# Performance work log

Measured on AMD Instinct MI355X. Metric: run time of the kernel, lower is better.

## Reference

```python
import jax, jax.numpy as jnp
import numpy as np

B, C, H, W = 2, 256, 56, 56
NH = 8
HD = C // NH
SCALE = HD ** -0.5
BN_EPS = 1e-5


def _linear(x, w, b=None):
    y = jnp.einsum('...i,oi->...o', x, w)
    return y + b if b is not None else y


def _dwconv3(v, w, b):
    # depthwise 3x3, stride 1, pad 1
    y = jax.lax.conv_general_dilated(v, w, (1, 1), 'SAME',
                                     dimension_numbers=('NCHW', 'OIHW', 'NCHW'),
                                     feature_group_count=C)
    return y + b[None, :, None, None]


def _spectral(x, context, qw, kvw, pw, pb, dww, dwb):
    # SpectralCrossAttention, sr_ratio=1 path
    xt = jnp.transpose(x, (0, 2, 3, 1))                    # B,H,W,C
    q = jnp.transpose(_linear(xt, qw), (0, 3, 1, 2))       # B,C,H,W
    ct = jnp.transpose(context, (0, 2, 3, 1))
    kv = _linear(ct, kvw)                                  # B,H,W,2C -> split [2,C]
    k = jnp.transpose(kv[..., :C], (0, 3, 1, 2))
    v = jnp.transpose(kv[..., C:], (0, 3, 1, 2))
    v_local = _dwconv3(v, dww, dwb)
    qf = jnp.fft.rfft2(q, s=(H, W), axes=(-2, -1), norm='ortho')
    kf = jnp.fft.rfft2(k, s=(H, W), axes=(-2, -1), norm='ortho')
    attn_map = jnp.fft.irfft2(qf * kf, s=(H, W), axes=(-2, -1), norm='ortho')
    out = attn_map * v + v_local
    out = _linear(jnp.transpose(out, (0, 2, 3, 1)), pw, pb)
    return jnp.transpose(out, (0, 3, 1, 2))


def _token(x, context, qw, kvw, pw, pb, cw):
    # TokenSpectralResidualCrossAttention, sr_ratio=1 path (de_conv = Identity)
    N = H * W
    xt = jnp.transpose(x.reshape(B, C, N), (0, 2, 1))       # B,N,C
    ct = jnp.transpose(context.reshape(B, C, N), (0, 2, 1))
    q = jnp.transpose(_linear(xt, qw).reshape(B, N, NH, HD), (0, 2, 1, 3))  # B,NH,N,HD
    kv = _linear(ct, kvw).reshape(B, N, 2, NH, HD)
    k = jnp.transpose(kv[:, :, 0], (0, 2, 1, 3))
    v = jnp.transpose(kv[:, :, 1], (0, 2, 1, 3))            # B,NH,N,HD
    attn = jax.nn.softmax(jnp.einsum('bhnd,bhmd->bhnm', q, k) * SCALE, axis=-1)
    x_attn = jnp.transpose(jnp.einsum('bhnm,bhmd->bhnd', attn, v), (0, 2, 1, 3)).reshape(B, N, C)
    v_img = jnp.transpose(v, (0, 1, 3, 2)).reshape(B, C, H, W)
    vf = jnp.fft.rfft2(v_img, s=(H, W), axes=(-2, -1), norm='ortho')
    weight = cw[..., 0] + 1j * cw[..., 1]                   # C,H,W//2+1 complex
    v_res = jnp.fft.irfft2(vf * weight[None], s=(H, W), axes=(-2, -1), norm='ortho')
    v_res = jnp.transpose(v_res.reshape(B, C, N), (0, 2, 1))
    out = _linear(x_attn + v_res, pw, pb)
    return jnp.transpose(out, (0, 2, 1)).reshape(B, C, H, W)


def _fuse(os_, ot, g_w1, g_bn_g, g_bn_b, g_w2, g_b2):
    # spatial_gate: Conv1x1(2C->C, no bias) -> BN(eval: mean0/var1) -> ReLU -> Conv1x1(C->1) -> Sigmoid
    g_in = jnp.concatenate([os_, ot], axis=1)               # B,2C,H,W
    h = jnp.einsum('oc,bchw->bohw', g_w1, g_in)
    h = h / jnp.sqrt(1.0 + BN_EPS) * g_bn_g[None, :, None, None] + g_bn_b[None, :, None, None]
    h = jax.nn.relu(h)
    gate = jax.nn.sigmoid(jnp.einsum('oc,bchw->bohw', g_w2, h) + g_b2[None, :, None, None])
    return gate * os_ + (1.0 - gate) * ot


def setup_inputs():
    key = jax.random.key(0)
    ks = jax.random.split(key, 14)
    p = lambda i, shape, s=0.02: jax.random.normal(ks[i], shape, jnp.float32) * s
    return {
        'x': jax.random.normal(ks[0], (B, C, H, W), jnp.float32),
        'context': jax.random.normal(ks[1], (B, C, H, W), jnp.float32),
        's_q_w': p(2, (C, C)),
        's_kv_w': p(3, (2 * C, C)),
        's_proj_w': p(4, (C, C)),
        's_proj_b': jnp.zeros((C,), jnp.float32),
        's_dw_w': p(5, (C, 1, 3, 3), float(np.sqrt(2.0 / 9.0))),
        's_dw_b': jnp.zeros((C,), jnp.float32),
        't_q_w': p(6, (C, C)),
        't_kv_w': p(7, (2 * C, C)),
        't_proj_w': p(8, (C, C)),
        't_proj_b': jnp.zeros((C,), jnp.float32),
        't_cw': p(9, (C, H, W // 2 + 1, 2)),
        'g_w1': p(10, (C, 2 * C), float(np.sqrt(2.0 / C))),
        'g_bn_g': jnp.ones((C,), jnp.float32),
        'g_bn_b': jnp.zeros((C,), jnp.float32),
        'g_w2': p(11, (1, C), float(np.sqrt(2.0 / C))),
        'g_b2': jnp.zeros((1,), jnp.float32),
    }


def reference(x, context, s_q_w, s_kv_w, s_proj_w, s_proj_b, s_dw_w, s_dw_b,
              t_q_w, t_kv_w, t_proj_w, t_proj_b, t_cw,
              g_w1, g_bn_g, g_bn_b, g_w2, g_b2):
    os_ = _spectral(x, context, s_q_w, s_kv_w, s_proj_w, s_proj_b, s_dw_w, s_dw_b)
    ot = _token(x, context, t_q_w, t_kv_w, t_proj_w, t_proj_b, t_cw)
    return _fuse(os_, ot, g_w1, g_bn_g, g_bn_b, g_w2, g_b2)
```

## Files before the change

kernel.cpp:

```cpp
#include <hip/hip_runtime.h>

namespace {
constexpr int kB = 2;
constexpr int kC = 256;
constexpr int kH = 56;
constexpr int kW = 56;
constexpr int kN = kH * kW;
constexpr int kNH = 8;
constexpr int kHD = 32;
constexpr int kNF = kW / 2 + 1;
constexpr int kSpec = kH * kNF;
constexpr long kCN = (long)kC * kN;
constexpr float kAttScale = 0.17677669529663687f;
constexpr float kLog2e = 1.4426950408889634f;
constexpr float kAng = 6.283185307179586f / 56.0f;
constexpr int TW1F = 0;
constexpr int TW2F = 8192;
constexpr int TW1I = 12288;
constexpr int TW2I = 20480;
constexpr int TWTOT = 24576;
}

typedef __attribute__((ext_vector_type(8))) short short8;
typedef __attribute__((ext_vector_type(4))) float float4v;

union Frag {
    short8 s;
    unsigned short u[8];
    uint2 u2[2];
    uint4 u4;
};

__device__ __forceinline__ unsigned short f2b(float f) {
    unsigned u = __float_as_uint(f);
    return (unsigned short)((u + 0x7FFFu + ((u >> 16) & 1u)) >> 16);
}
__device__ __forceinline__ unsigned f2b_pk(float a, float b) {
    unsigned ua = __float_as_uint(a); ua = (ua + 0x7FFFu + ((ua >> 16) & 1u)) >> 16;
    unsigned ub = __float_as_uint(b); ub = (ub + 0x7FFFu + ((ub >> 16) & 1u)) >> 16;
    return ua | (ub << 16);
}
__device__ __forceinline__ unsigned pk_trunc(float a, float b) {
    return (__float_as_uint(a) >> 16) | (__float_as_uint(b) & 0xFFFF0000u);
}
__device__ __forceinline__ uint4 pk8(const float* v) {
    return make_uint4(f2b_pk(v[0], v[1]), f2b_pk(v[2], v[3]),
                      f2b_pk(v[4], v[5]), f2b_pk(v[6], v[7]));
}

__global__ __launch_bounds__(256)
void twiddle_init_kernel(unsigned short* __restrict__ tw)
{
    int idx = blockIdx.x * 256 + threadIdx.x;
    if (idx >= TWTOT) return;
    float val = 0.f;
    if (idx < TW2F) {
        int r = idx >> 6, c = idx & 63;
        if (c < 56) {
            if (r < 56)       val = cosf(kAng * (float)((r * c) % 56));
            else if (r < 112) val = sinf(kAng * (float)(((r - 56) * c) % 56));
        }
    } else if (idx < TW1I) {
        int t = idx - TW2F; int r = t >> 6, c = t & 63;
        if (c < 56) {
            if (r < 29)                  val = cosf(kAng * (float)((r * c) % 56));
            else if (r >= 32 && r < 61)  val = sinf(kAng * (float)(((r - 32) * c) % 56));
        }
    } else if (idx < TW2I) {
        int t = idx - TW1I; int r = t >> 6, c = t & 63;
        if (c < 56) {
            if (r < 56)                  val = cosf(kAng * (float)((r * c) % 56));
            else if (r >= 64 && r < 120) val = sinf(kAng * (float)(((r - 64) * c) % 56));
        }
    } else {
        int t = idx - TW2I; int x = t >> 6, c = t & 63;
        if (x < 56 && c < 58) {
            int v = c >> 1;
            float wv = ((v == 0) || (v == 28)) ? 1.f : 2.f;
            float a = kAng * (float)((v * x) % 56);
            val = (c & 1) ? (-wv * sinf(a)) : (wv * cosf(a));
        }
    }
    tw[idx] = f2b(val);
}

__device__ void dft_fwd_body(char* smem, int bx,
                             const float* __restrict__ s0, const float* __restrict__ s1,
                             const float* __restrict__ s2, float* __restrict__ d0,
                             float* __restrict__ d1, float* __restrict__ d2,
                             const unsigned short* __restrict__ tw)
{
    const int which = bx >> 9, ch = bx & 511;
    const int b = ch >> 8, c = ch & 255;
    const float* src; long stride; float* spec;
    if (which == 0)      { src = s0; stride = kCN;     spec = d0; }
    else if (which == 1) { src = s1; stride = 2 * kCN; spec = d1; }
    else                 { src = s2; stride = 2 * kCN; spec = d2; }
    const float* img = src + (long)b * stride + (long)c * kN;

    unsigned short (*Gb)[72]   = (unsigned short(*)[72])smem;
    unsigned short (*imgT)[72] = (unsigned short(*)[72])(smem + 18432);
    float (*Yb)[116]           = (float(*)[116])(smem + 18432);

    const int tid = threadIdx.x;
    const int wave = tid >> 6, lane = tid & 63;
    const int ln = lane & 15, qd = lane >> 4;

    for (int i = tid; i < 64 * 72; i += 256) {
        int r = i / 72, cc = i - r * 72;
        if (r >= 56 || cc >= 56) imgT[r][cc] = 0;
    }
    for (int i = tid; i < kN; i += 256) {
        int y = i / 56, x = i - y * 56;
        imgT[x][y] = f2b(img[i]);
    }
    __syncthreads();

    float4v acc1[2][4];
#pragma unroll
    for (int m = 0; m < 2; ++m)
#pragma unroll
        for (int n = 0; n < 4; ++n) acc1[m][n] = (float4v){0.f, 0.f, 0.f, 0.f};
#pragma unroll
    for (int ks = 0; ks < 2; ++ks) {
        Frag a[2], bf[4];
#pragma unroll
        for (int m = 0; m < 2; ++m)
            a[m].u4 = *(const uint4*)(tw + TW1F + ((2 * wave + m) * 16 + ln) * 64 + ks * 32 + qd * 8);
#pragma unroll
        for (int n = 0; n < 4; ++n)
            bf[n].u4 = *(const uint4*)&imgT[n * 16 + ln][ks * 32 + qd * 8];
#pragma unroll
        for (int m = 0; m < 2; ++m)
#pragma unroll
            for (int n = 0; n < 4; ++n)
                acc1[m][n] = __builtin_amdgcn_mfma_f32_16x16x32_bf16(a[m].s, bf[n].s, acc1[m][n], 0, 0, 0);
    }
#pragma unroll
    for (int m = 0; m < 2; ++m)
#pragma unroll
        for (int n = 0; n < 4; ++n)
#pragma unroll
            for (int r = 0; r < 4; ++r)
                Gb[(2 * wave + m) * 16 + qd * 4 + r][n * 16 + ln] = f2b(acc1[m][n][r]);
    __syncthreads();

    float4v acc2[7];
#pragma unroll
    for (int n = 0; n < 7; ++n) acc2[n] = (float4v){0.f, 0.f, 0.f, 0.f};
#pragma unroll
    for (int ks = 0; ks < 2; ++ks) {
        Frag a;
        a.u4 = *(const uint4*)(tw + TW2F + (wave * 16 + ln) * 64 + ks * 32 + qd * 8);
#pragma unroll
        for (int n = 0; n < 7; ++n) {
            Frag bb;
            bb.u4 = *(const uint4*)&Gb[n * 16 + ln][ks * 32 + qd * 8];
            acc2[n] = __builtin_amdgcn_mfma_f32_16x16x32_bf16(a.s, bb.s, acc2[n], 0, 0, 0);
        }
    }
#pragma unroll
    for (int n = 0; n < 7; ++n)
#pragma unroll
        for (int r = 0; r < 4; ++r)
            Yb[wave * 16 + qd * 4 + r][n * 16 + ln] = acc2[n][r];
    __syncthreads();

    float2* outp = (float2*)spec + (long)ch * kSpec;
    for (int i = tid; i < kSpec; i += 256) {
        int u = i / kNF, v = i - u * kNF;
        float Qr = Yb[v][u] - Yb[32 + v][56 + u];
        float Qi = -Yb[32 + v][u] - Yb[v][56 + u];
        outp[i] = make_float2(Qr, Qi);
    }
}

__device__ void prepack_body(char* smem, int blk, const float* __restrict__ tkv,
                             unsigned short* __restrict__ Kp,
                             unsigned short* __restrict__ Vp)
{
    const int i = blk % 49;
    const int h = (blk / 49) & 7;
    const int b = blk / (49 * 8);
    const float* kb = tkv + (long)b * 2 * kCN + (long)h * kHD * kN;
    const float* vb = kb + kCN;
    const int tid = threadIdx.x;

    float (*Ks)[72] = (float(*)[72])smem;
#pragma unroll
    for (int j = 0; j < 8; ++j) {
        int e = tid + j * 256;
        int d = e >> 6, c = e & 63;
        Ks[d][c] = kb[(long)d * kN + i * 64 + c];
    }
    __syncthreads();
    {
        int tl = tid >> 6, lnn = (tid >> 2) & 15, qdd = tid & 3;
        float v[8];
#pragma unroll
        for (int j = 0; j < 8; ++j) v[j] = Ks[qdd * 8 + j][tl * 16 + lnn];
        unsigned short* dst = Kp + ((long)(b * 8 + h) * 196 + 4 * i + tl) * 512 + lnn * 32 + qdd * 8;
        *(uint4*)dst = pk8(v);
    }
    {
        int g = tid >> 7, dh = (tid >> 6) & 1, lnn = (tid >> 2) & 15, qdd = tid & 3;
        int d = dh * 16 + lnn;
        const float* src = vb + (long)d * kN + i * 64 + g * 32 + qdd * 8;
        float v[8];
        *(float4*)&v[0] = *(const float4*)src;
        *(float4*)&v[4] = *(const float4*)(src + 4);
        unsigned short* dst = Vp + ((long)(b * 8 + h) * 49 + i) * 2048 + ((g * 2 + dh) * 16 + lnn) * 32 + qdd * 8;
        *(uint4*)dst = pk8(v);
    }
}

__global__ __launch_bounds__(256)
void fwd3_prepack_kernel(const float* __restrict__ s0, const float* __restrict__ s1,
                         const float* __restrict__ s2, float* __restrict__ d0,
                         float* __restrict__ d1, float* __restrict__ d2,
                         const unsigned short* __restrict__ tw,
                         const float* __restrict__ tkv,
                         unsigned short* __restrict__ Kp, unsigned short* __restrict__ Vp)
{
    __shared__ __align__(16) char smem[48128];
    if (blockIdx.x < 1536)
        dft_fwd_body(smem, blockIdx.x, s0, s1, s2, d0, d1, d2, tw);
    else
        prepack_body(smem, blockIdx.x - 1536, tkv, Kp, Vp);
}

__global__ __launch_bounds__(256)
void dft_inv_mfma2(const float* __restrict__ fQ, const float* __restrict__ fK,
                   const float* __restrict__ fV, const float* __restrict__ cw,
                   float* __restrict__ dst1, float* __restrict__ dst2,
                   const float* __restrict__ skvp, const float* __restrict__ dww,
                   const float* __restrict__ dwb, const unsigned short* __restrict__ tw)
{
    const int unit = blockIdx.x >> 9;
    const int ch = blockIdx.x & 511;
    const int b = ch >> 8, c = ch & 255;
    __shared__ __align__(16) char smem[41984];
    unsigned short (*Pb)[72] = (unsigned short(*)[72])smem;
    float (*Yb)[64]          = (float(*)[64])(smem + 9216);
    unsigned short (*T2)[72] = (unsigned short(*)[72])smem;
    float (*svs)[65]         = (float(*)[65])(smem + 9216);

    const int tid = threadIdx.x;
    const int wave = tid >> 6, lane = tid & 63;
    const int ln = lane & 15, qd = lane >> 4;

    const float2* Pin; const float2* Min; float scale; float* dst;
    if (unit == 0) {
        Pin = (const float2*)fQ + (long)ch * kSpec;
        Min = (const float2*)fK + (long)ch * kSpec;
        scale = 1.0f / 175616.0f; dst = dst1;
    } else {
        Pin = (const float2*)fV + (long)ch * kSpec;
        Min = (const float2*)cw + (long)c * kSpec;
        scale = 1.0f / 3136.0f; dst = dst2;
    }

    for (int i = tid; i < 64 * 72; i += 256) {
        int r = i / 72, cc = i - r * 72;
        if (r >= 58 || cc >= 56) Pb[r][cc] = 0;
    }
    for (int i = tid; i < kSpec; i += 256) {
        int u = i / kNF, v = i - u * kNF;
        float2 p = Pin[i];
        float2 m = Min[i];
        float pr = (p.x * m.x - p.y * m.y) * scale;
        float pi = (p.x * m.y + p.y * m.x) * scale;
        Pb[2 * v][u]     = f2b(pr);
        Pb[2 * v + 1][u] = f2b(pi);
    }
    __syncthreads();

    float4v acc1[2][4];
#pragma unroll
    for (int m = 0; m < 2; ++m)
#pragma unroll
        for (int n = 0; n < 4; ++n) acc1[m][n] = (float4v){0.f, 0.f, 0.f, 0.f};
#pragma unroll
    for (int ks = 0; ks < 2; ++ks) {
        Frag a[2], bf[4];
#pragma unroll
        for (int m = 0; m < 2; ++m)
            a[m].u4 = *(const uint4*)(tw + TW1I + ((2 * wave + m) * 16 + ln) * 64 + ks * 32 + qd * 8);
#pragma unroll
        for (int n = 0; n < 4; ++n)
            bf[n].u4 = *(const uint4*)&Pb[n * 16 + ln][ks * 32 + qd * 8];
#pragma unroll
        for (int m = 0; m < 2; ++m)
#pragma unroll
            for (int n = 0; n < 4; ++n)
                acc1[m][n] = __builtin_amdgcn_mfma_f32_16x16x32_bf16(a[m].s, bf[n].s, acc1[m][n], 0, 0, 0);
    }
#pragma unroll
    for (int m = 0; m < 2; ++m)
#pragma unroll
        for (int n = 0; n < 4; ++n)
#pragma unroll
            for (int r = 0; r < 4; ++r)
                Yb[(2 * wave + m) * 16 + qd * 4 + r][n * 16 + ln] = acc1[m][n][r];
    __syncthreads();

    for (int i = tid; i < 64 * 72; i += 256) {
        int r = i / 72, cc = i - r * 72;
        if (r >= 56 || cc >= 58) T2[r][cc] = 0;
    }
    __syncthreads();
    for (int i = tid; i < 56 * kNF; i += 256) {
        int y = i / kNF, v = i - y * kNF;
        float Tr = Yb[y][2 * v]     - Yb[64 + y][2 * v + 1];
        float Ti = Yb[y][2 * v + 1] + Yb[64 + y][2 * v];
        T2[y][2 * v]     = f2b(Tr);
        T2[y][2 * v + 1] = f2b(Ti);
    }
    __syncthreads();

    float wreg[9]; float bias = 0.f;
    if (unit == 0) {
        const float* svp = skvp + (long)b * 2 * kCN + kCN + (long)c * kN;
        for (int i = tid; i < 58 * 65; i += 256) {
            int y = i / 65, x = i - y * 65;
            if (y == 0 || y == 57 || x == 0 || x >= 57) ((float*)svs)[i] = 0.f;
        }
        for (int i = tid; i < kN; i += 256) {
            int y = i / 56, x = i - y * 56;
            svs[y + 1][x + 1] = svp[i];
        }
#pragma unroll
        for (int j = 0; j < 9; ++j) wreg[j] = dww[c * 9 + j];
        bias = dwb[c];
    }

    float4v acc2[4];
#pragma unroll
    for (int n = 0; n < 4; ++n) acc2[n] = (float4v){0.f, 0.f, 0.f, 0.f};
#pragma unroll
    for (int ks = 0; ks < 2; ++ks) {
        Frag a;
        a.u4 = *(const uint4*)(tw + TW2I + (wave * 16 + ln) * 64 + ks * 32 + qd * 8);
#pragma unroll
        for (int n = 0; n < 4; ++n) {
            Frag bb;
            bb.u4 = *(const uint4*)&T2[n * 16 + ln][ks * 32 + qd * 8];
            acc2[n] = __builtin_amdgcn_mfma_f32_16x16x32_bf16(a.s, bb.s, acc2[n], 0, 0, 0);
        }
    }
    __syncthreads();

    float* outd = dst + (long)ch * kN;
#pragma unroll
    for (int n = 0; n < 4; ++n) {
        int y = n * 16 + ln;
        if (y < 56) {
#pragma unroll
            for (int r = 0; r < 4; ++r) {
                int x = wave * 16 + qd * 4 + r;
                if (x < 56) {
                    int e = y * 56 + x;
                    if (unit == 0) {
                        float s = bias;
                        s = fmaf(wreg[0], svs[y][x],     s);
                        s = fmaf(wreg[1], svs[y][x + 1], s);
                        s = fmaf(wreg[2], svs[y][x + 2], s);
                        s = fmaf(wreg[3], svs[y + 1][x],     s);
                        s = fmaf(wreg[4], svs[y + 1][x + 1], s);
                        s = fmaf(wreg[5], svs[y + 1][x + 2], s);
                        s = fmaf(wreg[6], svs[y + 2][x],     s);
                        s = fmaf(wreg[7], svs[y + 2][x + 1], s);
                        s = fmaf(wreg[8], svs[y + 2][x + 2], s);
                        outd[e] = fmaf(acc2[n][r], svs[y + 1][x + 1], s);
                    } else {
                        outd[e] = acc2[n][r];
                    }
                }
            }
        }
    }
}

__global__ __launch_bounds__(256)
void gemm_fused(const float* __restrict__ W0, const float* __restrict__ W1,
                const float* __restrict__ X0, const float* __restrict__ X1,
                const float* __restrict__ b0, const float* __restrict__ b1,
                float* __restrict__ Y0, float* __restrict__ Y1,
                int oHalf, int CI, long xbs, long ybs, int oOffset)
{
    const int b  = blockIdx.z;
    const int sel = blockIdx.y >= oHalf;
    const int o0 = (sel ? blockIdx.y - oHalf : blockIdx.y) * 64;
    const int oY = o0 + (sel ? oOffset : 0);
    const int n0 = blockIdx.x * 128;
    const float* Wm = sel ? W1 : W0;
    const float* bias = sel ? b1 : b0;
    const float* Xb = (sel ? X1 : X0) + (long)b * xbs;
    float* Yb = (sel ? Y1 : Y0) + (long)b * ybs;

    __shared__ __align__(16) unsigned short Wt[64][40];
    __shared__ __align__(16) unsigned short Xt[128][40];

    const int tid = threadIdx.x;
    const int wave = tid >> 6, lane = tid & 63;
    const int ln = lane & 15, qd = lane >> 4;
    const int wy = wave >> 1, wx = wave & 1;

    const int ow = tid >> 2, kcw = tid & 3;
    const int nx = tid & 127, kcx = tid >> 7;
    const bool xvalid = (n0 + nx) < kN;

    float4v acc[2][4];
#pragma unroll
    for (int i = 0; i < 2; ++i)
#pragma unroll
        for (int j = 0; j < 4; ++j) acc[i][j] = (float4v){0.f, 0.f, 0.f, 0.f};

    float wpre[8], xpre[16];
    {
        const float* ws = Wm + (long)(o0 + ow) * CI + kcw * 8;
        *(float4*)&wpre[0] = *(const float4*)ws;
        *(float4*)&wpre[4] = *(const float4*)(ws + 4);
#pragma unroll
        for (int j = 0; j < 16; ++j)
            xpre[j] = xvalid ? Xb[(long)(kcx * 16 + j) * kN + n0 + nx] : 0.f;
    }

    for (int k0 = 0; k0 < CI; k0 += 32) {
        *(uint4*)&Wt[ow][kcw * 8]      = pk8(wpre);
        *(uint4*)&Xt[nx][kcx * 16]     = pk8(xpre);
        *(uint4*)&Xt[nx][kcx * 16 + 8] = pk8(xpre + 8);
        __syncthreads();

        if (k0 + 32 < CI) {
            const float* ws = Wm + (long)(o0 + ow) * CI + k0 + 32 + kcw * 8;
            *(float4*)&wpre[0] = *(const float4*)ws;
            *(float4*)&wpre[4] = *(const float4*)(ws + 4);
#pragma unroll
            for (int j = 0; j < 16; ++j)
                xpre[j] = xvalid ? Xb[(long)(k0 + 32 + kcx * 16 + j) * kN + n0 + nx] : 0.f;
        }

        Frag af[2], bf4[4];
#pragma unroll
        for (int mt = 0; mt < 2; ++mt)
            af[mt].u4 = *(const uint4*)&Wt[wy * 32 + mt * 16 + ln][qd * 8];
#pragma unroll
        for (int nt = 0; nt < 4; ++nt)
            bf4[nt].u4 = *(const uint4*)&Xt[wx * 64 + nt * 16 + ln][qd * 8];
#pragma unroll
        for (int mt = 0; mt < 2; ++mt)
#pragma unroll
            for (int nt = 0; nt < 4; ++nt)
                acc[mt][nt] = __builtin_amdgcn_mfma_f32_16x16x32_bf16(
                    af[mt].s, bf4[nt].s, acc[mt][nt], 0, 0, 0);
        __syncthreads();
    }

#pragma unroll
    for (int mt = 0; mt < 2; ++mt) {
        const int obL = o0 + wy * 32 + mt * 16 + qd * 4;
        const int obY = oY + wy * 32 + mt * 16 + qd * 4;
#pragma unroll
        for (int nt = 0; nt < 4; ++nt) {
            const int n = n0 + wx * 64 + nt * 16 + ln;
            if (n < kN) {
#pragma unroll
                for (int r = 0; r < 4; ++r) {
                    float v = acc[mt][nt][r];
                    if (bias) v += bias[obL + r];
                    Yb[(long)(obY + r) * kN + n] = v;
                }
            }
        }
    }
}

__global__ __launch_bounds__(256)
void gemm_bn_kernel(const float* __restrict__ Wm, const float* __restrict__ X,
                    const float* __restrict__ gamma, const float* __restrict__ beta,
                    float* __restrict__ Y, int CI, long xbs, long ybs)
{
    const int b  = blockIdx.z;
    const int o0 = blockIdx.y * 64;
    const int n0 = blockIdx.x * 128;
    const float* Xb = X + (long)b * xbs;
    float* Yb = Y + (long)b * ybs;

    __shared__ __align__(16) unsigned short Wt[64][40];
    __shared__ __align__(16) unsigned short Xt[128][40];

    const int tid = threadIdx.x;
    const int wave = tid >> 6, lane = tid & 63;
    const int ln = lane & 15, qd = lane >> 4;
    const int wy = wave >> 1, wx = wave & 1;

    const int ow = tid >> 2, kcw = tid & 3;
    const int nx = tid & 127, kcx = tid >> 7;
    const bool xvalid = (n0 + nx) < kN;

    float4v acc[2][4];
#pragma unroll
    for (int i = 0; i < 2; ++i)
#pragma unroll
        for (int j = 0; j < 4; ++j) acc[i][j] = (float4v){0.f, 0.f, 0.f, 0.f};

    float wpre[8], xpre[16];
    {
        const float* ws = Wm + (long)(o0 + ow) * CI + kcw * 8;
        *(float4*)&wpre[0] = *(const float4*)ws;
        *(float4*)&wpre[4] = *(const float4*)(ws + 4);
#pragma unroll
        for (int j = 0; j < 16; ++j)
            xpre[j] = xvalid ? Xb[(long)(kcx * 16 + j) * kN + n0 + nx] : 0.f;
    }

    for (int k0 = 0; k0 < CI; k0 += 32) {
        *(uint4*)&Wt[ow][kcw * 8]      = pk8(wpre);
        *(uint4*)&Xt[nx][kcx * 16]     = pk8(xpre);
        *(uint4*)&Xt[nx][kcx * 16 + 8] = pk8(xpre + 8);
        __syncthreads();

        if (k0 + 32 < CI) {
            const float* ws = Wm + (long)(o0 + ow) * CI + k0 + 32 + kcw * 8;
            *(float4*)&wpre[0] = *(const float4*)ws;
            *(float4*)&wpre[4] = *(const float4*)(ws + 4);
#pragma unroll
            for (int j = 0; j < 16; ++j)
                xpre[j] = xvalid ? Xb[(long)(k0 + 32 + kcx * 16 + j) * kN + n0 + nx] : 0.f;
        }

        Frag af[2], bf4[4];
#pragma unroll
        for (int mt = 0; mt < 2; ++mt)
            af[mt].u4 = *(const uint4*)&Wt[wy * 32 + mt * 16 + ln][qd * 8];
#pragma unroll
        for (int nt = 0; nt < 4; ++nt)
            bf4[nt].u4 = *(const uint4*)&Xt[wx * 64 + nt * 16 + ln][qd * 8];
#pragma unroll
        for (int mt = 0; mt < 2; ++mt)
#pragma unroll
            for (int nt = 0; nt < 4; ++nt)
                acc[mt][nt] = __builtin_amdgcn_mfma_f32_16x16x32_bf16(
                    af[mt].s, bf4[nt].s, acc[mt][nt], 0, 0, 0);
        __syncthreads();
    }

    const float rs = rsqrtf(1.0f + 1e-5f);
#pragma unroll
    for (int mt = 0; mt < 2; ++mt) {
        const int ob = o0 + wy * 32 + mt * 16 + qd * 4;
#pragma unroll
        for (int nt = 0; nt < 4; ++nt) {
            const int n = n0 + wx * 64 + nt * 16 + ln;
            if (n < kN) {
#pragma unroll
                for (int r = 0; r < 4; ++r) {
                    const int o = ob + r;
                    float v = fmaxf(fmaf(acc[mt][nt][r], gamma[o] * rs, beta[o]), 0.f);
                    Yb[(long)o * kN + n] = v;
                }
            }
        }
    }
}

__global__ __launch_bounds__(256, 4)
void attn_mfma_kernel(const float* __restrict__ tq,
                      const unsigned short* __restrict__ Kp,
                      const unsigned short* __restrict__ Vp,
                      float* __restrict__ Op, float* __restrict__ lp)
{
    const int b = blockIdx.z >> 2, sp = blockIdx.z & 3;
    const int h = blockIdx.y;
    const int q0 = blockIdx.x * 128;
    const int tid = threadIdx.x;
    const int wave = tid >> 6, lane = tid & 63;
    const int qd = lane >> 4, ln = lane & 15;
    const int i0 = (sp == 0) ? 0 : (12 * sp + 1);
    const int i1 = 12 * sp + 13;

    const float* qb = tq + (long)b * kCN + (long)h * kHD * kN;
    const unsigned short* KpB = Kp + (long)(b * 8 + h) * 196 * 512 + ln * 32 + qd * 8;
    const unsigned short* VpB = Vp + (long)(b * 8 + h) * 49 * 2048 + ln * 32 + qd * 8;

    __shared__ __align__(16) unsigned short Ps[4][32 * 40];
    unsigned short* PsW = Ps[wave];

    const float qscale = kAttScale * kLog2e;
    Frag qf[2];
#pragma unroll
    for (int qt = 0; qt < 2; ++qt) {
        int qg = q0 + wave * 32 + qt * 16 + ln;
        bool qv = qg < kN;
#pragma unroll
        for (int j = 0; j < 8; ++j) {
            int d = qd * 8 + j;
            float v = qv ? qb[(long)d * kN + qg] * qscale : 0.f;
            qf[qt].u[j] = f2b(v);
        }
    }

    float4v o[2][2];
#pragma unroll
    for (int qt = 0; qt < 2; ++qt)
#pragma unroll
        for (int dh = 0; dh < 2; ++dh) o[qt][dh] = (float4v){0.f, 0.f, 0.f, 0.f};
    float lsum[2] = {0.f, 0.f};

    unsigned W[4][2][2];
    Frag ka[4];
#pragma unroll
    for (int m = 0; m < 4; ++m)
        ka[m].u4 = *(const uint4*)(KpB + (long)(4 * i0 + m) * 512);

    auto computeW = [&]() {
#pragma unroll
        for (int m = 0; m < 4; ++m) {
            float4v s0 = __builtin_amdgcn_mfma_f32_16x16x32_bf16(
                ka[m].s, qf[0].s, (float4v){0.f, 0.f, 0.f, 0.f}, 0, 0, 0);
            float4v s1 = __builtin_amdgcn_mfma_f32_16x16x32_bf16(
                ka[m].s, qf[1].s, (float4v){0.f, 0.f, 0.f, 0.f}, 0, 0, 0);
            float a0 = __builtin_amdgcn_exp2f(s0[0]);
            float a1 = __builtin_amdgcn_exp2f(s0[1]);
            float a2 = __builtin_amdgcn_exp2f(s0[2]);
            float a3 = __builtin_amdgcn_exp2f(s0[3]);
            lsum[0] += (a0 + a1) + (a2 + a3);
            W[m][0][0] = pk_trunc(a0, a1);
            W[m][0][1] = pk_trunc(a2, a3);
            float b0 = __builtin_amdgcn_exp2f(s1[0]);
            float b1 = __builtin_amdgcn_exp2f(s1[1]);
            float b2 = __builtin_amdgcn_exp2f(s1[2]);
            float b3 = __builtin_amdgcn_exp2f(s1[3]);
            lsum[1] += (b0 + b1) + (b2 + b3);
            W[m][1][0] = pk_trunc(b0, b1);
            W[m][1][1] = pk_trunc(b2, b3);
        }
    };

    computeW();
    if (i0 + 1 < i1) {
#pragma unroll
        for (int m = 0; m < 4; ++m)
            ka[m].u4 = *(const uint4*)(KpB + (long)(4 * (i0 + 1) + m) * 512);
    }

    for (int i = i0; i < i1; ++i) {
        Frag va[2][2];
#pragma unroll
        for (int g = 0; g < 2; ++g)
#pragma unroll
            for (int dh = 0; dh < 2; ++dh)
                va[g][dh].u4 = *(const uint4*)(VpB + (long)i * 2048 + (g * 2 + dh) * 512);

#pragma unroll
        for (int m = 0; m < 4; ++m)
#pragma unroll
            for (int qt = 0; qt < 2; ++qt)
                *(uint2*)&PsW[(qt * 16 + ln) * 40 + m * 16 + qd * 4] =
                    make_uint2(W[m][qt][0], W[m][qt][1]);

        if (i + 1 < i1) {
            computeW();
            if (i + 2 < i1) {
#pragma unroll
                for (int m = 0; m < 4; ++m)
                    ka[m].u4 = *(const uint4*)(KpB + (long)(4 * (i + 2) + m) * 512);
            }
        }

#pragma unroll
        for (int g = 0; g < 2; ++g) {
            Frag pa[2];
#pragma unroll
            for (int qt = 0; qt < 2; ++qt)
                pa[qt].u4 = *(const uint4*)&PsW[(qt * 16 + ln) * 40 + g * 32 + qd * 8];
#pragma unroll
            for (int qt = 0; qt < 2; ++qt)
#pragma unroll
                for (int dh = 0; dh < 2; ++dh)
                    o[qt][dh] = __builtin_amdgcn_mfma_f32_16x16x32_bf16(
                        pa[qt].s, va[g][dh].s, o[qt][dh], 0, 0, 0);
        }
    }

    const long grp = (long)(sp * 16 + b * 8 + h);
#pragma unroll
    for (int qt = 0; qt < 2; ++qt) {
        lsum[qt] += __shfl_xor(lsum[qt], 16, 64);
        lsum[qt] += __shfl_xor(lsum[qt], 32, 64);
        if (qd == 0)
            lp[grp * 3200 + q0 + wave * 32 + qt * 16 + ln] = lsum[qt];
#pragma unroll
        for (int dh = 0; dh < 2; ++dh)
#pragma unroll
            for (int r = 0; r < 4; ++r) {
                int q = q0 + wave * 32 + qt * 16 + qd * 4 + r;
                Op[(grp * 3200 + q) * 32 + dh * 16 + ln] = o[qt][dh][r];
            }
    }
}

__global__ __launch_bounds__(256)
void attn_combine_kernel(const float* __restrict__ Op, const float* __restrict__ lp,
                         float* __restrict__ xo)
{
    const int qc = blockIdx.x, bh = blockIdx.y;
    const int b = bh >> 3, h = bh & 7;
    const int q0 = qc * 64;
    __shared__ float T[32][65];
    const int tid = threadIdx.x;

    for (int i = tid; i < 64 * 32; i += 256) {
        int ql = i >> 5, d = i & 31;
        float ov = 0.f, l = 0.f;
#pragma unroll
        for (int s = 0; s < 4; ++s) {
            long g = (long)(s * 16 + bh);
            ov += Op[(g * 3200 + q0 + ql) * 32 + d];
            l  += lp[g * 3200 + q0 + ql];
        }
        T[d][ql] = ov / l;
    }
    __syncthreads();
    for (int i = tid; i < 32 * 64; i += 256) {
        int d = i >> 6, ql = i & 63;
        xo[(long)b * kCN + (long)(h * kHD + d) * kN + q0 + ql] += T[d][ql];
    }
}

__global__ __launch_bounds__(256)
void gateblend_kernel(const float* __restrict__ hbuf, const float* __restrict__ w2,
                      const float* __restrict__ b2, const float* __restrict__ gcat,
                      float* __restrict__ out)
{
    const int n0 = blockIdx.x * 64;
    const int b = blockIdx.y;
    const int lane = threadIdx.x & 63;
    const int g = threadIdx.x >> 6;
    const float* hb = hbuf + (long)b * kCN + n0 + lane;
    float s = 0.f;
#pragma unroll 8
    for (int c = g * 64; c < g * 64 + 64; ++c)
        s = fmaf(w2[c], hb[(long)c * kN], s);
    __shared__ float red[4][64];
    __shared__ float sgate[64];
    red[g][lane] = s;
    __syncthreads();
    if (g == 0) {
        float t = red[0][lane] + red[1][lane] + red[2][lane] + red[3][lane];
        sgate[lane] = 1.f / (1.f + __expf(-(t + b2[0])));
    }
    __syncthreads();
    const float gt = sgate[lane];
    const float* osp = gcat + (long)b * 2 * kCN + n0 + lane;
    const float* otp = osp + kCN;
    float* op = out + (long)b * kCN + n0 + lane;
    for (int c = g; c < kC; c += 4) {
        float os = osp[(long)c * kN];
        float ot = otp[(long)c * kN];
        op[(long)c * kN] = gt * os + (1.f - gt) * ot;
    }
}

extern "C" void kernel_launch(void* const* d_in, const int* in_sizes, int n_in,
                              void* d_out, int out_size, void* d_ws, size_t ws_size,
                              hipStream_t stream)
{
    const float* x      = (const float*)d_in[0];
    const float* ctx    = (const float*)d_in[1];
    const float* s_q_w  = (const float*)d_in[2];
    const float* s_kv_w = (const float*)d_in[3];
    const float* s_p_w  = (const float*)d_in[4];
    const float* s_p_b  = (const float*)d_in[5];
    const float* s_dw_w = (const float*)d_in[6];
    const float* s_dw_b = (const float*)d_in[7];
    const float* t_q_w  = (const float*)d_in[8];
    const float* t_kv_w = (const float*)d_in[9];
    const float* t_p_w  = (const float*)d_in[10];
    const float* t_p_b  = (const float*)d_in[11];
    const float* t_cw   = (const float*)d_in[12];
    const float* g_w1   = (const float*)d_in[13];
    const float* g_bn_g = (const float*)d_in[14];
    const float* g_bn_b = (const float*)d_in[15];
    const float* g_w2   = (const float*)d_in[16];
    const float* g_b2   = (const float*)d_in[17];
    float* out = (float*)d_out;

    float* ws = (float*)d_ws;
    const long SPEC2 = (long)kB * kC * kSpec * 2;
    float* sq   = ws;
    float* skv  = sq   + kB * kCN;
    float* tq   = skv  + kB * 2 * kCN;
    float* tkv  = tq   + kB * kCN;
    float* vloc = tkv  + kB * 2 * kCN;
    float* fQ   = vloc + kB * kCN;
    float* fK   = fQ   + SPEC2;
    float* fV   = fK   + SPEC2;
    float* gcat = fV   + SPEC2;
    float* gate = gcat + kB * 2 * kCN;
    unsigned short* tw = (unsigned short*)(gate + kB * kN);
    unsigned short* Kp = tw + TWTOT;
    unsigned short* Vp = Kp + (long)16 * 196 * 512;
    float* Opart = (float*)(Vp + (long)16 * 49 * 2048);
    float* lpart = Opart + (long)64 * 3200 * 32;

    dim3 blk(256, 1, 1);

    twiddle_init_kernel<<<dim3(TWTOT / 256), blk, 0, stream>>>(tw);

    gemm_fused<<<dim3(25, 8, kB), blk, 0, stream>>>(
        s_q_w, t_q_w, x, x, nullptr, nullptr, sq, tq, 4, kC, kCN, kCN, 0);
    gemm_fused<<<dim3(25, 16, kB), blk, 0, stream>>>(
        s_kv_w, t_kv_w, ctx, ctx, nullptr, nullptr, skv, tkv, 8, kC, kCN, 2 * kCN, 0);

    fwd3_prepack_kernel<<<dim3(3 * kB * kC + kB * kNH * 49), blk, 0, stream>>>(
        sq, skv, tkv + kCN, fQ, fK, fV, tw, tkv, Kp, Vp);

    dft_inv_mfma2<<<dim3(2 * kB * kC), blk, 0, stream>>>(
        fQ, fK, fV, t_cw, vloc, sq, skv, s_dw_w, s_dw_b, tw);

    attn_mfma_kernel<<<dim3(25, kNH, 4 * kB), blk, 0, stream>>>(tq, Kp, Vp, Opart, lpart);
    attn_combine_kernel<<<dim3(49, 16), blk, 0, stream>>>(Opart, lpart, sq);

    gemm_fused<<<dim3(25, 8, kB), blk, 0, stream>>>(
        s_p_w, t_p_w, vloc, sq, s_p_b, t_p_b, gcat, gcat, 4, kC, kCN, 2 * kCN, 256);

    gemm_bn_kernel<<<dim3(25, 4, kB), blk, 0, stream>>>(g_w1, gcat, g_bn_g, g_bn_b, tkv, 2 * kC, 2 * kCN, kCN);
    gateblend_kernel<<<dim3(49, kB), blk, 0, stream>>>(tkv, g_w2, g_b2, gcat, out);
}
```

Measured before the change: 281.5 us.

## Store DFT intermediates in LDS as bf16 and remap attention blocks per XCD

The forward and inverse DFT kernels now keep their intermediate Yb tiles in shared memory as bf16 instead of fp32. This shrinks the static LDS allocation so more blocks can be resident per CU. Separately, the attention kernel's 3D grid is flattened to 1D and remapped so that all blocks for one (batch, head) land on the same XCD, which should improve L2 reuse of that head's K/V. The cost is extra bf16 rounding of the DFT intermediates, which lowers precision.

```diff
diff --git a/kernel.cpp b/kernel.cpp
--- a/kernel.cpp
+++ b/kernel.cpp
@@ -35,6 +35,9 @@
     unsigned u = __float_as_uint(f);
     return (unsigned short)((u + 0x7FFFu + ((u >> 16) & 1u)) >> 16);
 }
+__device__ __forceinline__ float b2f(unsigned short u) {
+    return __uint_as_float((unsigned)u << 16);
+}
 __device__ __forceinline__ unsigned f2b_pk(float a, float b) {
     unsigned ua = __float_as_uint(a); ua = (ua + 0x7FFFu + ((ua >> 16) & 1u)) >> 16;
     unsigned ub = __float_as_uint(b); ub = (ub + 0x7FFFu + ((ub >> 16) & 1u)) >> 16;
@@ -98,9 +101,9 @@
     else                 { src = s2; stride = 2 * kCN; spec = d2; }
     const float* img = src + (long)b * stride + (long)c * kN;
 
-    unsigned short (*Gb)[72]   = (unsigned short(*)[72])smem;
-    unsigned short (*imgT)[72] = (unsigned short(*)[72])(smem + 18432);
-    float (*Yb)[116]           = (float(*)[116])(smem + 18432);
+    unsigned short (*Gb)[72]    = (unsigned short(*)[72])smem;
+    unsigned short (*imgT)[72]  = (unsigned short(*)[72])(smem + 18432);
+    unsigned short (*Yb)[116]   = (unsigned short(*)[116])(smem + 18432);
 
     const int tid = threadIdx.x;
     const int wave = tid >> 6, lane = tid & 63;
@@ -163,14 +166,14 @@
     for (int n = 0; n < 7; ++n)
 #pragma unroll
         for (int r = 0; r < 4; ++r)
-            Yb[wave * 16 + qd * 4 + r][n * 16 + ln] = acc2[n][r];
+            Yb[wave * 16 + qd * 4 + r][n * 16 + ln] = f2b(acc2[n][r]);
     __syncthreads();
 
     float2* outp = (float2*)spec + (long)ch * kSpec;
     for (int i = tid; i < kSpec; i += 256) {
         int u = i / kNF, v = i - u * kNF;
-        float Qr = Yb[v][u] - Yb[32 + v][56 + u];
-        float Qi = -Yb[32 + v][u] - Yb[v][56 + u];
+        float Qr = b2f(Yb[v][u]) - b2f(Yb[32 + v][56 + u]);
+        float Qi = -b2f(Yb[32 + v][u]) - b2f(Yb[v][56 + u]);
         outp[i] = make_float2(Qr, Qi);
     }
 }
@@ -222,7 +225,7 @@
                          const float* __restrict__ tkv,
                          unsigned short* __restrict__ Kp, unsigned short* __restrict__ Vp)
 {
-    __shared__ __align__(16) char smem[48128];
+    __shared__ __align__(16) char smem[33280];
     if (blockIdx.x < 1536)
         dft_fwd_body(smem, blockIdx.x, s0, s1, s2, d0, d1, d2, tw);
     else
@@ -239,11 +242,11 @@
     const int unit = blockIdx.x >> 9;
     const int ch = blockIdx.x & 511;
     const int b = ch >> 8, c = ch & 255;
-    __shared__ __align__(16) char smem[41984];
-    unsigned short (*Pb)[72] = (unsigned short(*)[72])smem;
-    float (*Yb)[64]          = (float(*)[64])(smem + 9216);
-    unsigned short (*T2)[72] = (unsigned short(*)[72])smem;
-    float (*svs)[65]         = (float(*)[65])(smem + 9216);
+    __shared__ __align__(16) char smem[27648];
+    unsigned short (*Pb)[72]  = (unsigned short(*)[72])smem;
+    unsigned short (*Yb)[72]  = (unsigned short(*)[72])(smem + 9216);
+    unsigned short (*T2)[72]  = (unsigned short(*)[72])smem;
+    float (*svs)[65]          = (float(*)[65])(smem + 9216);
 
     const int tid = threadIdx.x;
     const int wave = tid >> 6, lane = tid & 63;
@@ -301,7 +304,7 @@
         for (int n = 0; n < 4; ++n)
 #pragma unroll
             for (int r = 0; r < 4; ++r)
-                Yb[(2 * wave + m) * 16 + qd * 4 + r][n * 16 + ln] = acc1[m][n][r];
+                Yb[(2 * wave + m) * 16 + qd * 4 + r][n * 16 + ln] = f2b(acc1[m][n][r]);
     __syncthreads();
 
     for (int i = tid; i < 64 * 72; i += 256) {
@@ -311,8 +314,8 @@
     __syncthreads();
     for (int i = tid; i < 56 * kNF; i += 256) {
         int y = i / kNF, v = i - y * kNF;
-        float Tr = Yb[y][2 * v]     - Yb[64 + y][2 * v + 1];
-        float Ti = Yb[y][2 * v + 1] + Yb[64 + y][2 * v];
+        float Tr = b2f(Yb[y][2 * v])     - b2f(Yb[64 + y][2 * v + 1]);
+        float Ti = b2f(Yb[y][2 * v + 1]) + b2f(Yb[64 + y][2 * v]);
         T2[y][2 * v]     = f2b(Tr);
         T2[y][2 * v + 1] = f2b(Ti);
     }
@@ -571,9 +574,15 @@
                       const unsigned short* __restrict__ Vp,
                       float* __restrict__ Op, float* __restrict__ lp)
 {
-    const int b = blockIdx.z >> 2, sp = blockIdx.z & 3;
-    const int h = blockIdx.y;
-    const int q0 = blockIdx.x * 128;
+    const int bi = blockIdx.x;
+    const int xcd = bi & 7;
+    const int t = bi >> 3;
+    const int gsel = (t >= 100) ? 1 : 0;
+    const int r0 = t - gsel * 100;
+    const int grpId = (gsel << 3) | xcd;
+    const int b = grpId >> 3, h = grpId & 7;
+    const int sp = r0 / 25;
+    const int q0 = (r0 % 25) * 128;
     const int tid = threadIdx.x;
     const int wave = tid >> 6, lane = tid & 63;
     const int qd = lane >> 4, ln = lane & 15;
@@ -820,7 +829,7 @@
     dft_inv_mfma2<<<dim3(2 * kB * kC), blk, 0, stream>>>(
         fQ, fK, fV, t_cw, vloc, sq, skv, s_dw_w, s_dw_b, tw);
 
-    attn_mfma_kernel<<<dim3(25, kNH, 4 * kB), blk, 0, stream>>>(tq, Kp, Vp, Opart, lpart);
+    attn_mfma_kernel<<<dim3(1600), blk, 0, stream>>>(tq, Kp, Vp, Opart, lpart);
     attn_combine_kernel<<<dim3(49, 16), blk, 0, stream>>>(Opart, lpart, sq);
 
     gemm_fused<<<dim3(25, 8, kB), blk, 0, stream>>>(
```

Result: no change. 280.4 us (-0.4%).
